# Kernel tuning notes

Measured on AMD Instinct MI355X. Metric: run time of the kernel, lower is better.

## Reference

```python
import jax, jax.numpy as jnp
import numpy as np

N_HEADS = 16


def setup_inputs() -> dict:
    key = jax.random.key(0)
    ks = jax.random.split(key, 5)
    E = 1024
    x = jax.random.normal(ks[0], (2, 2048, E), dtype=jnp.float32)
    s = 1.0 / np.sqrt(E)
    Wq = jax.random.normal(ks[1], (E, E), dtype=jnp.float32) * s
    Wk = jax.random.normal(ks[2], (E, E), dtype=jnp.float32) * s
    Wv = jax.random.normal(ks[3], (E, E), dtype=jnp.float32) * s
    Wo = jax.random.normal(ks[4], (E, E), dtype=jnp.float32) * s
    bo = jnp.zeros((E,), dtype=jnp.float32)
    return {"x": x, "Wq": Wq, "Wk": Wk, "Wv": Wv, "Wo": Wo, "bo": bo}


def reference(x, Wq, Wk, Wv, Wo, bo):
    B, S, E = x.shape
    H = N_HEADS
    D = E // H
    # project and split heads: [B, H, S, D]
    def split_heads(y):
        return y.reshape(B, S, H, D).transpose(0, 2, 1, 3)
    q = split_heads(x @ Wq)
    k = split_heads(x @ Wk)
    v = split_heads(x @ Wv)
    # full score matrix [B, H, S, S]
    scores = jnp.einsum('bhqd,bhkd->bhqk', q, k)
    causal = jnp.triu(jnp.ones((S, S), dtype=bool), k=1)
    scores = jnp.where(causal, -jnp.inf, scores)
    attn = jax.nn.softmax(scores / jnp.sqrt(jnp.float32(D)), axis=-1)
    # dropout rate is 0.0 -> identity
    ctx = jnp.einsum('bhqk,bhkd->bhqd', attn, v)
    ctx = ctx.transpose(0, 2, 1, 3).reshape(B, S, E)
    return ctx @ Wo + bo
```

## Files before the change

### kernel.cpp

```cpp
#include <hip/hip_runtime.h>
#include <stdint.h>


#define N_HEADS 16
#define HD 64
#define SEQ 2048
#define EMB 1024

typedef __attribute__((ext_vector_type(8))) short s16x8;
typedef __attribute__((ext_vector_type(4))) float f32x4;

#define QSCALE 0.18033688f

__device__ __forceinline__ short f2b(float f) {
  union { float f; uint32_t u; } v; v.f = f;
  uint32_t u = v.u;
  u += 0x7fffu + ((u >> 16) & 1u);
  return (short)(u >> 16);
}

__device__ __forceinline__ uint32_t pk2(float a, float b) {
  union { float f; uint32_t u; } x, y; x.f = a; y.f = b;
  return ((x.u + 0x8000u) >> 16) | ((y.u + 0x8000u) & 0xffff0000u);
}

__device__ __forceinline__ float exp2a(float x) {
  float r; asm("v_exp_f32 %0, %1" : "=v"(r) : "v"(x)); return r;
}

__device__ __forceinline__ void gll16(const void* g, void* l) {
  __builtin_amdgcn_global_load_lds((const __attribute__((address_space(1))) void*)g,
                                   (__attribute__((address_space(3))) void*)l, 16, 0, 0);
}

#define SWZ(row, chunk) ((((row) * 8) + ((chunk) ^ ((row) & 7))) * 8)

__global__ __launch_bounds__(256) void k_prep(const float* __restrict__ x,
                                              const float* __restrict__ W0,
                                              const float* __restrict__ W1,
                                              const float* __restrict__ W2,
                                              const float* __restrict__ W3,
                                              short* __restrict__ xb,
                                              short* __restrict__ wt) {
  const int z = blockIdx.x, t = threadIdx.x;
  if (z < 4096) {
    int i = z * 256 + t;
    float4 v = ((const float4*)x)[i];
    short4 o;
    o.x = f2b(v.x); o.y = f2b(v.y); o.z = f2b(v.z); o.w = f2b(v.w);
    ((short4*)xb)[i] = o;
  } else {
    __shared__ float tile[32][33];
    int bz = z - 4096;
    int w = bz >> 10, rem = bz & 1023;
    int bn = (rem & 31) * 32, bk = (rem >> 5) * 32;
    const float* W = w == 0 ? W0 : w == 1 ? W1 : w == 2 ? W2 : W3;
    short* o = wt + (size_t)w * EMB * EMB;
    int tx = t & 31, ty = t >> 5;
    for (int i = ty; i < 32; i += 8)
      tile[i][tx] = W[(size_t)(bk + i) * EMB + bn + tx];
    __syncthreads();
    for (int i = ty; i < 32; i += 8)
      o[(size_t)(bn + i) * EMB + bk + tx] = f2b(tile[tx][i]);
  }
}

template <int MODE, int MT>
__global__ __launch_bounds__(256) void k_gemm(const short* __restrict__ A,
                                              const short* __restrict__ BT,
                                              void* __restrict__ outp,
                                              const float* __restrict__ bias) {
  constexpr int BM = MT * 32;
  constexpr bool SWAP = (MODE != 2);
  constexpr bool DBUF = (MODE == 1);
  constexpr int NB = DBUF ? 2 : 1;
  constexpr int MAIN = NB * (BM * 32 + 128 * 32);
  constexpr int EPIL = (MODE == 1) ? 0 : 128 * 132;
  constexpr int SMSZ = MAIN > EPIL ? MAIN : EPIL;
  __shared__ alignas(16) short smem[SMSZ];

  const int t = threadIdx.x;
  const int m0 = blockIdx.x * BM;
  const int n0 = blockIdx.y * 128;
  const int wave = t >> 6, lane = t & 63;
  const int wm = (wave >> 1) * (MT * 16), wn = (wave & 1) * 64;
  const int ml = lane & 15, quad = lane >> 4;
  const int k0 = quad * 8;
  const int lr = lane >> 2, lc = (lane & 3) * 8;

  auto stage = [&](int kb, int p) {
    short* as = smem + p * (BM * 32);
    short* bs = smem + NB * (BM * 32) + p * (128 * 32);
#pragma unroll
    for (int rr = 0; rr < MT / 2; rr++) {
      int arow = wave * (MT * 8) + rr * 16;
      gll16(A + (size_t)(m0 + arow + lr) * EMB + kb + lc, &as[arow * 32]);
    }
#pragma unroll
    for (int rr = 0; rr < 2; rr++) {
      int brow = wave * 32 + rr * 16;
      gll16(BT + (size_t)(n0 + brow + lr) * EMB + kb + lc, &bs[brow * 32]);
    }
  };

  f32x4 acc[MT][4] = {};
  int pb = 0;

  if (DBUF) stage(0, 0);
  for (int kb = 0; kb < EMB; kb += 32) {
    __syncthreads();
    if (DBUF) {
      if (kb + 32 < EMB) stage(kb + 32, pb ^ 1);
    } else {
      stage(kb, 0);
      __syncthreads();
    }
    const short* as = smem + (DBUF ? pb : 0) * (BM * 32);
    const short* bs = smem + NB * (BM * 32) + (DBUF ? pb : 0) * (128 * 32);
    s16x8 af[MT], bf[4];
#pragma unroll
    for (int i = 0; i < MT; i++) af[i] = *(const s16x8*)&as[(wm + i * 16 + ml) * 32 + k0];
#pragma unroll
    for (int i = 0; i < 4; i++) bf[i] = *(const s16x8*)&bs[(wn + i * 16 + ml) * 32 + k0];
#pragma unroll
    for (int mt = 0; mt < MT; mt++)
#pragma unroll
      for (int nt = 0; nt < 4; nt++)
        acc[mt][nt] = SWAP
          ? __builtin_amdgcn_mfma_f32_16x16x32_bf16(bf[nt], af[mt], acc[mt][nt], 0, 0, 0)
          : __builtin_amdgcn_mfma_f32_16x16x32_bf16(af[mt], bf[nt], acc[mt][nt], 0, 0, 0);
    pb ^= 1;
  }

  if (MODE == 0) {
    __syncthreads();
    short* Vls = smem;
    const int wsel = blockIdx.y >> 3;
    const float qs = (wsel == 0) ? QSCALE : 1.0f;
    const int n0l = (blockIdx.y & 7) * 128;
#pragma unroll
    for (int mt = 0; mt < MT; mt++) {
      int mr = wm + mt * 16 + ml;
#pragma unroll
      for (int nt = 0; nt < 4; nt++) {
        uint2 w;
        w.x = pk2(acc[mt][nt][0] * qs, acc[mt][nt][1] * qs);
        w.y = pk2(acc[mt][nt][2] * qs, acc[mt][nt][3] * qs);
        *(uint2*)&Vls[mr * 132 + wn + nt * 16 + quad * 4] = w;
      }
    }
    __syncthreads();
    short* ob = (short*)outp + (size_t)wsel * (4u * 1024 * 1024);
    const int bb = m0 >> 11, ss0 = m0 & (SEQ - 1);
#pragma unroll
    for (int i = 0; i < 8; i++) {
      int mrow = i * 16 + (t >> 4);
      int ncol = (t & 15) * 8;
      int e = n0l + ncol, hh = e >> 6, dd = e & 63;
      *(uint4*)&ob[(((size_t)(bb * N_HEADS + hh) * SEQ) + ss0 + mrow) * 64 + dd] =
          *(const uint4*)&Vls[mrow * 132 + ncol];
    }
  } else if (MODE == 2) {
    __syncthreads();
    short* Vls = smem;
#pragma unroll
    for (int nt = 0; nt < 4; nt++) {
      int nl = wn + nt * 16 + ml;
#pragma unroll
      for (int mt = 0; mt < MT; mt++) {
        int mc = wm + mt * 16 + quad * 4;
        uint2 w;
        w.x = pk2(acc[mt][nt][0], acc[mt][nt][1]);
        w.y = pk2(acc[mt][nt][2], acc[mt][nt][3]);
        *(uint2*)&Vls[nl * 132 + mc] = w;
      }
    }
    __syncthreads();
    short* obv = (short*)outp + (size_t)8 * 1024 * 1024;
    const int e0 = n0;
    const int bb = m0 >> 11, ss0 = m0 & (SEQ - 1);
#pragma unroll
    for (int i = 0; i < 8; i++) {
      int nl = i * 16 + (t >> 4);
      int mc = (t & 15) * 8;
      int e = e0 + nl, hh = e >> 6, dd = e & 63;
      *(uint4*)&obv[((size_t)((bb * N_HEADS + hh) * HD + dd)) * SEQ + ss0 + mc] =
          *(const uint4*)&Vls[nl * 132 + mc];
    }
  } else {
    float* of = (float*)outp;
    f32x4 bv[4];
#pragma unroll
    for (int nt = 0; nt < 4; nt++)
      bv[nt] = *(const f32x4*)&bias[n0 + wn + nt * 16 + quad * 4];
#pragma unroll
    for (int mt = 0; mt < MT; mt++) {
      int mg = m0 + wm + mt * 16 + ml;
#pragma unroll
      for (int nt = 0; nt < 4; nt++) {
        f32x4 w = acc[mt][nt] + bv[nt];
        *(f32x4*)&of[(size_t)mg * EMB + n0 + wn + nt * 16 + quad * 4] = w;
      }
    }
  }
}

__global__ __launch_bounds__(256) void k_attn(const short* __restrict__ Q,
                                              const short* __restrict__ K,
                                              const short* __restrict__ Vt,
                                              short* __restrict__ ctx) {
  __shared__ alignas(16) short UQP[128 * 72];
  __shared__ alignas(16) short Ks0[64 * 64], Ks1[64 * 64];
  __shared__ alignas(16) short Vs0[64 * 64], Vs1[64 * 64];

  const int t = threadIdx.x, wave = t >> 6, lane = t & 63;
  const int ml = lane & 15, quad = lane >> 4;
  const int bh = blockIdx.y;
  const int qb = ((blockIdx.y >> 4) & 1) ? (15 - (int)blockIdx.x) : (int)blockIdx.x;
  const size_t base = (size_t)bh * SEQ * HD;
  const int q0 = qb * 128, wq = q0 + wave * 32;

  const int sr = lane >> 3;
  const int sc = ((lane & 7) ^ sr) * 8;

#pragma unroll
  for (int i = 0; i < 4; i++) {
    int r8 = wave * 32 + i * 8;
    gll16(Q + base + (size_t)(q0 + r8 + sr) * HD + sc, &UQP[r8 * 64]);
  }
  auto stageKV = [&](int kt, short* kd, short* vd) {
    const int kbase = kt * 64;
#pragma unroll
    for (int i = 0; i < 2; i++) {
      int r8 = wave * 16 + i * 8;
      gll16(K + base + (size_t)(kbase + r8 + sr) * HD + sc, &kd[r8 * 64]);
      gll16(Vt + base + (size_t)(r8 + sr) * SEQ + kbase + sc, &vd[r8 * 64]);
    }
  };

  f32x4 cacc[2][4] = {};
  float li[2] = {0.f, 0.f};
  short* Pw = &UQP[wave * 32 * 72];

  stageKV(0, Ks0, Vs0);
  __syncthreads();

  s16x8 qf[2][2];
#pragma unroll
  for (int s = 0; s < 2; s++)
#pragma unroll
    for (int c = 0; c < 2; c++)
      qf[s][c] = *(const s16x8*)&UQP[SWZ(wave * 32 + s * 16 + ml, 4 * c + quad)];
  __syncthreads();

  auto tile_body = [&](int kt, const short* kd, const short* vd) {
    const int kbase = kt * 64;
    if (kbase > wq + 31) return;
    const bool diag = (kbase + 63 > wq);
    f32x4 st[2][4];
#pragma unroll
    for (int nt = 0; nt < 4; nt++) {
      int row = nt * 16 + ml;
      s16x8 kf0 = *(const s16x8*)&kd[SWZ(row, quad)];
      s16x8 kf1 = *(const s16x8*)&kd[SWZ(row, 4 + quad)];
      f32x4 z0 = {};
      z0 = __builtin_amdgcn_mfma_f32_16x16x32_bf16(kf0, qf[0][0], z0, 0, 0, 0);
      st[0][nt] = __builtin_amdgcn_mfma_f32_16x16x32_bf16(kf1, qf[0][1], z0, 0, 0, 0);
      f32x4 z1 = {};
      z1 = __builtin_amdgcn_mfma_f32_16x16x32_bf16(kf0, qf[1][0], z1, 0, 0, 0);
      st[1][nt] = __builtin_amdgcn_mfma_f32_16x16x32_bf16(kf1, qf[1][1], z1, 0, 0, 0);
    }
#pragma unroll
    for (int s = 0; s < 2; s++) {
      const int qg = wq + s * 16 + ml;
      float rsum = 0.f;
#pragma unroll
      for (int nt = 0; nt < 4; nt++) {
        float p0 = exp2a(st[s][nt][0]);
        float p1 = exp2a(st[s][nt][1]);
        float p2 = exp2a(st[s][nt][2]);
        float p3 = exp2a(st[s][nt][3]);
        if (diag) {
          int kk = kbase + nt * 16 + quad * 4;
          if (kk + 0 > qg) p0 = 0.f;
          if (kk + 1 > qg) p1 = 0.f;
          if (kk + 2 > qg) p2 = 0.f;
          if (kk + 3 > qg) p3 = 0.f;
        }
        rsum += (p0 + p1) + (p2 + p3);
        uint2 w; w.x = pk2(p0, p1); w.y = pk2(p2, p3);
        *(uint2*)&Pw[(s * 16 + ml) * 72 + nt * 16 + quad * 4] = w;
      }
      li[s] += rsum;
    }
    __builtin_amdgcn_wave_barrier();

    s16x8 pf[2][2];
#pragma unroll
    for (int s = 0; s < 2; s++)
#pragma unroll
      for (int c = 0; c < 2; c++)
        pf[s][c] = *(const s16x8*)&Pw[(s * 16 + ml) * 72 + c * 32 + quad * 8];
#pragma unroll
    for (int mt = 0; mt < 4; mt++) {
      int row = mt * 16 + ml;
      s16x8 vf0 = *(const s16x8*)&vd[SWZ(row, quad)];
      s16x8 vf1 = *(const s16x8*)&vd[SWZ(row, 4 + quad)];
#pragma unroll
      for (int s = 0; s < 2; s++) {
        cacc[s][mt] = __builtin_amdgcn_mfma_f32_16x16x32_bf16(vf0, pf[s][0], cacc[s][mt], 0, 0, 0);
        cacc[s][mt] = __builtin_amdgcn_mfma_f32_16x16x32_bf16(vf1, pf[s][1], cacc[s][mt], 0, 0, 0);
      }
    }
  };

  const int nkt = 2 * qb + 2;
  for (int kt = 0; kt < nkt; kt += 2) {
    stageKV(kt + 1, Ks1, Vs1);
    tile_body(kt, Ks0, Vs0);
    __syncthreads();
    if (kt + 2 < nkt) stageKV(kt + 2, Ks0, Vs0);
    tile_body(kt + 1, Ks1, Vs1);
    __syncthreads();
  }

  float inv[2];
#pragma unroll
  for (int s = 0; s < 2; s++) {
    li[s] += __shfl_xor(li[s], 16, 64);
    li[s] += __shfl_xor(li[s], 32, 64);
    inv[s] = 1.0f / li[s];
  }
#pragma unroll
  for (int s = 0; s < 2; s++)
#pragma unroll
    for (int mt = 0; mt < 4; mt++) {
      uint2 w;
      w.x = pk2(cacc[s][mt][0] * inv[s], cacc[s][mt][1] * inv[s]);
      w.y = pk2(cacc[s][mt][2] * inv[s], cacc[s][mt][3] * inv[s]);
      *(uint2*)&Pw[(s * 16 + ml) * 72 + mt * 16 + quad * 4] = w;
    }
  __builtin_amdgcn_wave_barrier();
  const int b = bh >> 4, h = bh & 15;
  const int row = wave * 32 + (lane >> 1), c0 = (lane & 1) * 32;
  size_t gbase = ((size_t)(b * SEQ + q0 + row)) * EMB + h * 64 + c0;
#pragma unroll
  for (int i = 0; i < 4; i++)
    *(uint4*)&ctx[gbase + i * 8] = *(const uint4*)&UQP[row * 72 + c0 + i * 8];
}

extern "C" void kernel_launch(void* const* d_in, const int* in_sizes, int n_in,
                              void* d_out, int out_size, void* d_ws, size_t ws_size,
                              hipStream_t stream) {
  const float* x  = (const float*)d_in[0];
  const float* Wq = (const float*)d_in[1];
  const float* Wk = (const float*)d_in[2];
  const float* Wv = (const float*)d_in[3];
  const float* Wo = (const float*)d_in[4];
  const float* bo = (const float*)d_in[5];
  float* out = (float*)d_out;

  short* ws = (short*)d_ws;
  short* xb  = ws;
  short* wt  = ws + (size_t)4 * 1024 * 1024;
  short* qkv = ws + (size_t)8 * 1024 * 1024;

  k_prep<<<8192, 256, 0, stream>>>(x, Wq, Wk, Wv, Wo, xb, wt);
  k_gemm<0, 4><<<dim3(32, 16), 256, 0, stream>>>(xb, wt, qkv, nullptr);
  k_gemm<2, 4><<<dim3(32, 8), 256, 0, stream>>>(xb, wt + (size_t)2 * 1024 * 1024, qkv, nullptr);
  k_attn<<<dim3(16, 32), 256, 0, stream>>>(qkv, qkv + (size_t)4 * 1024 * 1024,
                                           qkv + (size_t)8 * 1024 * 1024, xb);
  k_gemm<1, 2><<<dim3(64, 8), 256, 0, stream>>>(xb, wt + (size_t)3 * 1024 * 1024, out, bo);
}
```

Before: 195.6 us.

## Halve attention query tile to 64 rows and schedule heaviest blocks first

The attention kernel now processes 64 query rows per block (16 per wave) instead of 128, doubling the grid to 1024 blocks. Block ordering is changed so blockIdx.x indexes batch-head and the query block is reversed (31 - blockIdx.y), so the longest causal blocks are dispatched first. This replaces the previous zig-zag pairing as the load-balancing scheme. The aim is better occupancy and tail balance, at the cost of loading each K/V tile twice as often relative to the query work and less MFMA work per LDS load.

```diff
diff --git a/kernel.cpp b/kernel.cpp
--- a/kernel.cpp
+++ b/kernel.cpp
@@ -209,23 +209,23 @@
                                               const short* __restrict__ K,
                                               const short* __restrict__ Vt,
                                               short* __restrict__ ctx) {
-  __shared__ alignas(16) short UQP[128 * 72];
+  __shared__ alignas(16) short UQP[64 * 72];
   __shared__ alignas(16) short Ks0[64 * 64], Ks1[64 * 64];
   __shared__ alignas(16) short Vs0[64 * 64], Vs1[64 * 64];
 
   const int t = threadIdx.x, wave = t >> 6, lane = t & 63;
   const int ml = lane & 15, quad = lane >> 4;
-  const int bh = blockIdx.y;
-  const int qb = ((blockIdx.y >> 4) & 1) ? (15 - (int)blockIdx.x) : (int)blockIdx.x;
+  const int bh = blockIdx.x;
+  const int qb = 31 - (int)blockIdx.y;
   const size_t base = (size_t)bh * SEQ * HD;
-  const int q0 = qb * 128, wq = q0 + wave * 32;
+  const int q0 = qb * 64, wq = q0 + wave * 16;
 
   const int sr = lane >> 3;
   const int sc = ((lane & 7) ^ sr) * 8;
 
 #pragma unroll
-  for (int i = 0; i < 4; i++) {
-    int r8 = wave * 32 + i * 8;
+  for (int i = 0; i < 2; i++) {
+    int r8 = wave * 16 + i * 8;
     gll16(Q + base + (size_t)(q0 + r8 + sr) * HD + sc, &UQP[r8 * 64]);
   }
   auto stageKV = [&](int kt, short* kd, short* vd) {
@@ -238,115 +238,97 @@
     }
   };
 
-  f32x4 cacc[2][4] = {};
-  float li[2] = {0.f, 0.f};
-  short* Pw = &UQP[wave * 32 * 72];
+  f32x4 cacc[4] = {};
+  float li = 0.f;
+  short* Pw = &UQP[wave * 16 * 72];
 
   stageKV(0, Ks0, Vs0);
   __syncthreads();
 
-  s16x8 qf[2][2];
-#pragma unroll
-  for (int s = 0; s < 2; s++)
-#pragma unroll
-    for (int c = 0; c < 2; c++)
-      qf[s][c] = *(const s16x8*)&UQP[SWZ(wave * 32 + s * 16 + ml, 4 * c + quad)];
+  s16x8 qf[2];
+#pragma unroll
+  for (int c = 0; c < 2; c++)
+    qf[c] = *(const s16x8*)&UQP[SWZ(wave * 16 + ml, 4 * c + quad)];
   __syncthreads();
 
   auto tile_body = [&](int kt, const short* kd, const short* vd) {
     const int kbase = kt * 64;
-    if (kbase > wq + 31) return;
+    if (kbase > wq + 15) return;
     const bool diag = (kbase + 63 > wq);
-    f32x4 st[2][4];
+    f32x4 st[4];
 #pragma unroll
     for (int nt = 0; nt < 4; nt++) {
       int row = nt * 16 + ml;
       s16x8 kf0 = *(const s16x8*)&kd[SWZ(row, quad)];
       s16x8 kf1 = *(const s16x8*)&kd[SWZ(row, 4 + quad)];
-      f32x4 z0 = {};
-      z0 = __builtin_amdgcn_mfma_f32_16x16x32_bf16(kf0, qf[0][0], z0, 0, 0, 0);
-      st[0][nt] = __builtin_amdgcn_mfma_f32_16x16x32_bf16(kf1, qf[0][1], z0, 0, 0, 0);
-      f32x4 z1 = {};
-      z1 = __builtin_amdgcn_mfma_f32_16x16x32_bf16(kf0, qf[1][0], z1, 0, 0, 0);
-      st[1][nt] = __builtin_amdgcn_mfma_f32_16x16x32_bf16(kf1, qf[1][1], z1, 0, 0, 0);
-    }
-#pragma unroll
-    for (int s = 0; s < 2; s++) {
-      const int qg = wq + s * 16 + ml;
-      float rsum = 0.f;
-#pragma unroll
-      for (int nt = 0; nt < 4; nt++) {
-        float p0 = exp2a(st[s][nt][0]);
-        float p1 = exp2a(st[s][nt][1]);
-        float p2 = exp2a(st[s][nt][2]);
-        float p3 = exp2a(st[s][nt][3]);
-        if (diag) {
-          int kk = kbase + nt * 16 + quad * 4;
-          if (kk + 0 > qg) p0 = 0.f;
-          if (kk + 1 > qg) p1 = 0.f;
-          if (kk + 2 > qg) p2 = 0.f;
-          if (kk + 3 > qg) p3 = 0.f;
-        }
-        rsum += (p0 + p1) + (p2 + p3);
-        uint2 w; w.x = pk2(p0, p1); w.y = pk2(p2, p3);
-        *(uint2*)&Pw[(s * 16 + ml) * 72 + nt * 16 + quad * 4] = w;
+      f32x4 z = {};
+      z = __builtin_amdgcn_mfma_f32_16x16x32_bf16(kf0, qf[0], z, 0, 0, 0);
+      st[nt] = __builtin_amdgcn_mfma_f32_16x16x32_bf16(kf1, qf[1], z, 0, 0, 0);
+    }
+    const int qg = wq + ml;
+    float rsum = 0.f;
+#pragma unroll
+    for (int nt = 0; nt < 4; nt++) {
+      float p0 = exp2a(st[nt][0]);
+      float p1 = exp2a(st[nt][1]);
+      float p2 = exp2a(st[nt][2]);
+      float p3 = exp2a(st[nt][3]);
+      if (diag) {
+        int kk = kbase + nt * 16 + quad * 4;
+        if (kk + 0 > qg) p0 = 0.f;
+        if (kk + 1 > qg) p1 = 0.f;
+        if (kk + 2 > qg) p2 = 0.f;
+        if (kk + 3 > qg) p3 = 0.f;
       }
-      li[s] += rsum;
-    }
+      rsum += (p0 + p1) + (p2 + p3);
+      uint2 w; w.x = pk2(p0, p1); w.y = pk2(p2, p3);
+      *(uint2*)&Pw[ml * 72 + nt * 16 + quad * 4] = w;
+    }
+    li += rsum;
     __builtin_amdgcn_wave_barrier();
 
-    s16x8 pf[2][2];
-#pragma unroll
-    for (int s = 0; s < 2; s++)
-#pragma unroll
-      for (int c = 0; c < 2; c++)
-        pf[s][c] = *(const s16x8*)&Pw[(s * 16 + ml) * 72 + c * 32 + quad * 8];
+    s16x8 pf[2];
+#pragma unroll
+    for (int c = 0; c < 2; c++)
+      pf[c] = *(const s16x8*)&Pw[ml * 72 + c * 32 + quad * 8];
 #pragma unroll
     for (int mt = 0; mt < 4; mt++) {
       int row = mt * 16 + ml;
       s16x8 vf0 = *(const s16x8*)&vd[SWZ(row, quad)];
       s16x8 vf1 = *(const s16x8*)&vd[SWZ(row, 4 + quad)];
-#pragma unroll
-      for (int s = 0; s < 2; s++) {
-        cacc[s][mt] = __builtin_amdgcn_mfma_f32_16x16x32_bf16(vf0, pf[s][0], cacc[s][mt], 0, 0, 0);
-        cacc[s][mt] = __builtin_amdgcn_mfma_f32_16x16x32_bf16(vf1, pf[s][1], cacc[s][mt], 0, 0, 0);
-      }
+      cacc[mt] = __builtin_amdgcn_mfma_f32_16x16x32_bf16(vf0, pf[0], cacc[mt], 0, 0, 0);
+      cacc[mt] = __builtin_amdgcn_mfma_f32_16x16x32_bf16(vf1, pf[1], cacc[mt], 0, 0, 0);
     }
   };
 
-  const int nkt = 2 * qb + 2;
-  for (int kt = 0; kt < nkt; kt += 2) {
-    stageKV(kt + 1, Ks1, Vs1);
+  for (int kt = 0; kt <= qb; kt += 2) {
+    if (kt + 1 <= qb) stageKV(kt + 1, Ks1, Vs1);
     tile_body(kt, Ks0, Vs0);
     __syncthreads();
-    if (kt + 2 < nkt) stageKV(kt + 2, Ks0, Vs0);
-    tile_body(kt + 1, Ks1, Vs1);
-    __syncthreads();
-  }
-
-  float inv[2];
-#pragma unroll
-  for (int s = 0; s < 2; s++) {
-    li[s] += __shfl_xor(li[s], 16, 64);
-    li[s] += __shfl_xor(li[s], 32, 64);
-    inv[s] = 1.0f / li[s];
-  }
-#pragma unroll
-  for (int s = 0; s < 2; s++)
-#pragma unroll
-    for (int mt = 0; mt < 4; mt++) {
-      uint2 w;
-      w.x = pk2(cacc[s][mt][0] * inv[s], cacc[s][mt][1] * inv[s]);
-      w.y = pk2(cacc[s][mt][2] * inv[s], cacc[s][mt][3] * inv[s]);
-      *(uint2*)&Pw[(s * 16 + ml) * 72 + mt * 16 + quad * 4] = w;
-    }
+    if (kt + 2 <= qb) stageKV(kt + 2, Ks0, Vs0);
+    if (kt + 1 <= qb) tile_body(kt + 1, Ks1, Vs1);
+    __syncthreads();
+  }
+
+  li += __shfl_xor(li, 16, 64);
+  li += __shfl_xor(li, 32, 64);
+  float inv = 1.0f / li;
+#pragma unroll
+  for (int mt = 0; mt < 4; mt++) {
+    uint2 w;
+    w.x = pk2(cacc[mt][0] * inv, cacc[mt][1] * inv);
+    w.y = pk2(cacc[mt][2] * inv, cacc[mt][3] * inv);
+    *(uint2*)&Pw[ml * 72 + mt * 16 + quad * 4] = w;
+  }
   __builtin_amdgcn_wave_barrier();
   const int b = bh >> 4, h = bh & 15;
-  const int row = wave * 32 + (lane >> 1), c0 = (lane & 1) * 32;
-  size_t gbase = ((size_t)(b * SEQ + q0 + row)) * EMB + h * 64 + c0;
-#pragma unroll
-  for (int i = 0; i < 4; i++)
-    *(uint4*)&ctx[gbase + i * 8] = *(const uint4*)&UQP[row * 72 + c0 + i * 8];
+#pragma unroll
+  for (int i = 0; i < 2; i++) {
+    int row = i * 8 + (lane >> 3);
+    int q = wq + row;
+    size_t gbase = ((size_t)(b * SEQ + q)) * EMB + h * 64 + (lane & 7) * 8;
+    *(uint4*)&ctx[gbase] = *(const uint4*)&Pw[row * 72 + (lane & 7) * 8];
+  }
 }
 
 extern "C" void kernel_launch(void* const* d_in, const int* in_sizes, int n_in,
@@ -368,7 +350,7 @@
   k_prep<<<8192, 256, 0, stream>>>(x, Wq, Wk, Wv, Wo, xb, wt);
   k_gemm<0, 4><<<dim3(32, 16), 256, 0, stream>>>(xb, wt, qkv, nullptr);
   k_gemm<2, 4><<<dim3(32, 8), 256, 0, stream>>>(xb, wt + (size_t)2 * 1024 * 1024, qkv, nullptr);
-  k_attn<<<dim3(16, 32), 256, 0, stream>>>(qkv, qkv + (size_t)4 * 1024 * 1024,
+  k_attn<<<dim3(32, 32), 256, 0, stream>>>(qkv, qkv + (size_t)4 * 1024 * 1024,
                                            qkv + (size_t)8 * 1024 * 1024, xb);
   k_gemm<1, 2><<<dim3(64, 8), 256, 0, stream>>>(xb, wt + (size_t)3 * 1024 * 1024, out, bo);
 }
```

New measurement: 186.8 us. 4.5% less time.
